# Kernel optimization log

Measured on AMD Instinct MI355X. Metric: run time of the kernel, lower is better.

The kernel has to match this reference:

```python
import jax, jax.numpy as jnp
import numpy as np

# Distance grid for SK tables: uniform, 512 points on [1.0, 10.0] Bohr (typical SKF grid)
NGRID = 512
X0 = 1.0
XMAX = 10.0
DX = (XMAX - X0) / (NGRID - 1)

E_EDGES = 2_000_000
N_NODES = 500_000
N_BOND_TYPES = 10
NUM_INGRLS = 16   # idp_sk.reduced_matrix_element
N_ATOM_TYPES = 4
N_ONSITE = 4


def setup_inputs() -> dict:
    key = jax.random.key(0)
    k1, k2, k3, k4, k5, k6 = jax.random.split(key, 6)
    # edge lengths inside the table range [X0, XMAX)
    rij = X0 + jax.random.uniform(k1, (E_EDGES,), dtype=jnp.float32) * (XMAX - X0 - 0.1)
    edge_type = jax.random.randint(k2, (E_EDGES,), 0, N_BOND_TYPES, dtype=jnp.int32)
    atom_type = jax.random.randint(k3, (N_NODES,), 0, N_ATOM_TYPES, dtype=jnp.int32)
    hopping_tables = jax.random.normal(k4, (N_BOND_TYPES, NUM_INGRLS, NGRID), dtype=jnp.float32)
    overlap_tables = jax.random.normal(k5, (N_BOND_TYPES, NUM_INGRLS, NGRID), dtype=jnp.float32)
    onsiteE = jax.random.normal(k6, (N_ATOM_TYPES, N_ONSITE), dtype=jnp.float32)
    return {"rij": rij, "edge_type": edge_type, "atom_type": atom_type,
            "hopping_tables": hopping_tables, "overlap_tables": overlap_tables,
            "onsiteE": onsiteE}


def _interp_tables(tables, etype, r):
    """1D linear interpolation (HoppingIntp method='linear'), vectorized over
    ALL edges at once instead of the per-bond-type masked loop.
    tables: [B, M, G]; etype: [E] int; r: [E] float -> [E, M]."""
    t = (r - X0) / DX
    i0 = jnp.clip(jnp.floor(t).astype(jnp.int32), 0, NGRID - 2)
    frac = (t - i0.astype(r.dtype))[:, None]          # [E, 1]
    y0 = tables[etype, :, i0]                          # [E, M] gather
    y1 = tables[etype, :, i0 + 1]                      # [E, M] gather
    return y0 * (1.0 - frac) + y1 * frac


def reference(rij, edge_type, atom_type, hopping_tables, overlap_tables, onsiteE):
    # edge SK hopping integrals: data[EDGE_FEATURES] = hopping_fn.get_skhij(rij, yy=hoptable)
    edge_features = _interp_tables(hopping_tables, edge_type, rij)     # [E, M]
    # edge SK overlap integrals (overlap=True branch)
    edge_overlap = _interp_tables(overlap_tables, edge_type, rij)      # [E, M]
    # onsite energies: onsite_fn.get_skEs(atomic_numbers) -> table lookup per atom
    node_features = onsiteE[atom_type]                                  # [N, n_onsite]
    return edge_features, edge_overlap, node_features
```

## Files before the change

kernel.cpp:

```cpp
#include <hip/hip_runtime.h>


#define NGRID 512
#define NUM_INGRLS 16
#define N_BOND_TYPES 10
#define PACKED_FLOATS (N_BOND_TYPES * NGRID * 32)
#define PACKED_BYTES  (PACKED_FLOATS * sizeof(float))

typedef float fx4 __attribute__((ext_vector_type(4)));

__global__ __launch_bounds__(256) void repack_tables(
    const float* __restrict__ hop,
    const float* __restrict__ ovl,
    float* __restrict__ packed)
{
    int t = blockIdx.x * blockDim.x + threadIdx.x;
    if (t >= N_BOND_TYPES * NGRID * NUM_INGRLS) return;
    int m = t & (NUM_INGRLS - 1);
    int g = (t >> 4) & (NGRID - 1);
    int b = t >> 13;
    float h = hop[((size_t)b * NUM_INGRLS + m) * NGRID + g];
    float o = ovl[((size_t)b * NUM_INGRLS + m) * NGRID + g];
    size_t row = ((size_t)b * NGRID + g) * 32;
    packed[row + m]      = h;
    packed[row + 16 + m] = o;
}

__global__ __launch_bounds__(256) void dftb_edge_packed_q(
    const float* __restrict__ rij,
    const int*   __restrict__ etype,
    const float* __restrict__ packed,
    float* __restrict__ out_hop,
    float* __restrict__ out_ovl,
    int E)
{
    const float X0f = 1.0f;
    const float DXf = (float)((10.0 - 1.0) / (NGRID - 1));

    int tid = blockIdx.x * blockDim.x + threadIdx.x;
    int e = tid >> 2;
    int q = tid & 3;
    if (e >= E) return;

    float r = rij[e];
    int   b = etype[e];

    float t  = (r - X0f) / DXf;
    int   i0 = (int)floorf(t);
    i0 = min(max(i0, 0), NGRID - 2);
    float frac = t - (float)i0;
    float w0   = 1.0f - frac;

    const fx4* row = (const fx4*)(packed + ((size_t)b * NGRID + i0) * 32);
    fx4 h0 = row[q];
    fx4 o0 = row[4 + q];
    fx4 h1 = row[8 + q];
    fx4 o1 = row[12 + q];

    fx4 hv = h0 * w0 + h1 * frac;
    fx4 ov = o0 * w0 + o1 * frac;

    size_t slot = (size_t)e * 4 + q;
    __builtin_nontemporal_store(hv, (fx4*)out_hop + slot);
    __builtin_nontemporal_store(ov, (fx4*)out_ovl + slot);
}

__global__ __launch_bounds__(256) void dftb_edge_kernel(
    const float* __restrict__ rij,
    const int*   __restrict__ etype,
    const float* __restrict__ hop,
    const float* __restrict__ ovl,
    float* __restrict__ out_hop,
    float* __restrict__ out_ovl,
    int E)
{
    const float X0f = 1.0f;
    const float DXf = (float)((10.0 - 1.0) / (NGRID - 1));

    int e = blockIdx.x * blockDim.x + threadIdx.x;
    if (e >= E) return;

    float r = rij[e];
    int   b = etype[e];

    float t  = (r - X0f) / DXf;
    int   i0 = (int)floorf(t);
    i0 = min(max(i0, 0), NGRID - 2);
    float frac = t - (float)i0;
    float w0   = 1.0f - frac;

    const float* hbase = hop + (size_t)b * (NUM_INGRLS * NGRID) + i0;
    const float* obase = ovl + (size_t)b * (NUM_INGRLS * NGRID) + i0;

    float oh[NUM_INGRLS];
    float oo[NUM_INGRLS];
#pragma unroll
    for (int m = 0; m < NUM_INGRLS; ++m) {
        float y0 = hbase[m * NGRID];
        float y1 = hbase[m * NGRID + 1];
        oh[m] = y0 * w0 + y1 * frac;
        float z0 = obase[m * NGRID];
        float z1 = obase[m * NGRID + 1];
        oo[m] = z0 * w0 + z1 * frac;
    }

    float4* oh4 = (float4*)(out_hop + (size_t)e * NUM_INGRLS);
    float4* oo4 = (float4*)(out_ovl + (size_t)e * NUM_INGRLS);
#pragma unroll
    for (int qq = 0; qq < 4; ++qq) {
        oh4[qq] = make_float4(oh[4*qq+0], oh[4*qq+1], oh[4*qq+2], oh[4*qq+3]);
        oo4[qq] = make_float4(oo[4*qq+0], oo[4*qq+1], oo[4*qq+2], oo[4*qq+3]);
    }
}

__global__ __launch_bounds__(256) void dftb_node_kernel(
    const int*   __restrict__ atype,
    const float* __restrict__ onsiteE,
    float* __restrict__ out,
    int N)
{
    int n = blockIdx.x * blockDim.x + threadIdx.x;
    if (n >= N) return;
    int a = atype[n];
    const float4* src = (const float4*)onsiteE;
    ((float4*)out)[n] = src[a];
}

extern "C" void kernel_launch(void* const* d_in, const int* in_sizes, int n_in,
                              void* d_out, int out_size, void* d_ws, size_t ws_size,
                              hipStream_t stream) {
    const float* rij       = (const float*)d_in[0];
    const int*   edge_type = (const int*)  d_in[1];
    const int*   atom_type = (const int*)  d_in[2];
    const float* hop_tab   = (const float*)d_in[3];
    const float* ovl_tab   = (const float*)d_in[4];
    const float* onsiteE   = (const float*)d_in[5];

    const int E = in_sizes[0];
    const int N = in_sizes[2];

    float* out_hop  = (float*)d_out;
    float* out_ovl  = out_hop + (size_t)E * NUM_INGRLS;
    float* out_node = out_ovl + (size_t)E * NUM_INGRLS;

    if (d_ws != nullptr && ws_size >= PACKED_BYTES) {
        float* packed = (float*)d_ws;
        {
            int total = N_BOND_TYPES * NGRID * NUM_INGRLS;
            dim3 block(256);
            dim3 grid((total + 255) / 256);
            repack_tables<<<grid, block, 0, stream>>>(hop_tab, ovl_tab, packed);
        }
        {
            long long total = 4LL * E;
            dim3 block(256);
            dim3 grid((unsigned)((total + 255) / 256));
            dftb_edge_packed_q<<<grid, block, 0, stream>>>(
                rij, edge_type, packed, out_hop, out_ovl, E);
        }
    } else {
        dim3 block(256);
        dim3 grid((E + 255) / 256);
        dftb_edge_kernel<<<grid, block, 0, stream>>>(
            rij, edge_type, hop_tab, ovl_tab, out_hop, out_ovl, E);
    }

    {
        dim3 block(256);
        dim3 grid((N + 255) / 256);
        dftb_node_kernel<<<grid, block, 0, stream>>>(
            atom_type, onsiteE, out_node, N);
    }
}
```

Baseline: 305.2 us.

## Pack SK tables as fp16 with adjacent grid endpoints per row

Repacks hopping and overlap tables into fp16 with each integral's g and g+1 values for both tables stored together. Each edge then fetches one contiguous row instead of two float rows. Work is split across 8 threads per edge with 2-float stores. The aim is to cut gather traffic and table footprint, at the cost of fp16 precision in the interpolated tables and narrower stores.

```diff
diff --git a/kernel.cpp b/kernel.cpp
--- a/kernel.cpp
+++ b/kernel.cpp
@@ -4,32 +4,40 @@
 #define NGRID 512
 #define NUM_INGRLS 16
 #define N_BOND_TYPES 10
-#define PACKED_FLOATS (N_BOND_TYPES * NGRID * 32)
-#define PACKED_BYTES  (PACKED_FLOATS * sizeof(float))
+#define PACK2_HALFS (N_BOND_TYPES * NGRID * NUM_INGRLS * 4)
+#define PACK2_BYTES (PACK2_HALFS * 2)
 
-typedef float fx4 __attribute__((ext_vector_type(4)));
+typedef float    fx4 __attribute__((ext_vector_type(4)));
+typedef float    fx2 __attribute__((ext_vector_type(2)));
+typedef _Float16 hx4 __attribute__((ext_vector_type(4)));
+typedef _Float16 hx8 __attribute__((ext_vector_type(8)));
 
-__global__ __launch_bounds__(256) void repack_tables(
+__global__ __launch_bounds__(256) void repack_tables_p2(
     const float* __restrict__ hop,
     const float* __restrict__ ovl,
-    float* __restrict__ packed)
+    _Float16* __restrict__ packed)
 {
     int t = blockIdx.x * blockDim.x + threadIdx.x;
     if (t >= N_BOND_TYPES * NGRID * NUM_INGRLS) return;
     int m = t & (NUM_INGRLS - 1);
     int g = (t >> 4) & (NGRID - 1);
     int b = t >> 13;
-    float h = hop[((size_t)b * NUM_INGRLS + m) * NGRID + g];
-    float o = ovl[((size_t)b * NUM_INGRLS + m) * NGRID + g];
-    size_t row = ((size_t)b * NGRID + g) * 32;
-    packed[row + m]      = h;
-    packed[row + 16 + m] = o;
+    int g1 = min(g + 1, NGRID - 1);
+    const float* hb = hop + ((size_t)b * NUM_INGRLS + m) * NGRID;
+    const float* ob = ovl + ((size_t)b * NUM_INGRLS + m) * NGRID;
+    hx4 v;
+    v[0] = (_Float16)hb[g];
+    v[1] = (_Float16)hb[g1];
+    v[2] = (_Float16)ob[g];
+    v[3] = (_Float16)ob[g1];
+    size_t idx = (((size_t)b * NGRID + g) * NUM_INGRLS + m) * 4;
+    *(hx4*)(packed + idx) = v;
 }
 
-__global__ __launch_bounds__(256) void dftb_edge_packed_q(
+__global__ __launch_bounds__(256) void dftb_edge_p2(
     const float* __restrict__ rij,
     const int*   __restrict__ etype,
-    const float* __restrict__ packed,
+    const _Float16* __restrict__ packed,
     float* __restrict__ out_hop,
     float* __restrict__ out_ovl,
     int E)
@@ -38,8 +46,8 @@
     const float DXf = (float)((10.0 - 1.0) / (NGRID - 1));
 
     int tid = blockIdx.x * blockDim.x + threadIdx.x;
-    int e = tid >> 2;
-    int q = tid & 3;
+    int e = tid >> 3;
+    int l = tid & 7;
     if (e >= E) return;
 
     float r = rij[e];
@@ -51,18 +59,18 @@
     float frac = t - (float)i0;
     float w0   = 1.0f - frac;
 
-    const fx4* row = (const fx4*)(packed + ((size_t)b * NGRID + i0) * 32);
-    fx4 h0 = row[q];
-    fx4 o0 = row[4 + q];
-    fx4 h1 = row[8 + q];
-    fx4 o1 = row[12 + q];
+    const hx8* src = (const hx8*)(packed + ((size_t)b * NGRID + i0) * (NUM_INGRLS * 4)) + l;
+    hx8 v = *src;
 
-    fx4 hv = h0 * w0 + h1 * frac;
-    fx4 ov = o0 * w0 + o1 * frac;
+    fx2 hv, ov;
+    hv[0] = (float)v[0] * w0 + (float)v[1] * frac;
+    ov[0] = (float)v[2] * w0 + (float)v[3] * frac;
+    hv[1] = (float)v[4] * w0 + (float)v[5] * frac;
+    ov[1] = (float)v[6] * w0 + (float)v[7] * frac;
 
-    size_t slot = (size_t)e * 4 + q;
-    __builtin_nontemporal_store(hv, (fx4*)out_hop + slot);
-    __builtin_nontemporal_store(ov, (fx4*)out_ovl + slot);
+    size_t slot = (size_t)e * 8 + l;
+    __builtin_nontemporal_store(hv, (fx2*)out_hop + slot);
+    __builtin_nontemporal_store(ov, (fx2*)out_ovl + slot);
 }
 
 __global__ __launch_bounds__(256) void dftb_edge_kernel(
@@ -143,19 +151,19 @@
     float* out_ovl  = out_hop + (size_t)E * NUM_INGRLS;
     float* out_node = out_ovl + (size_t)E * NUM_INGRLS;
 
-    if (d_ws != nullptr && ws_size >= PACKED_BYTES) {
-        float* packed = (float*)d_ws;
+    if (d_ws != nullptr && ws_size >= PACK2_BYTES) {
+        _Float16* packed = (_Float16*)d_ws;
         {
             int total = N_BOND_TYPES * NGRID * NUM_INGRLS;
             dim3 block(256);
             dim3 grid((total + 255) / 256);
-            repack_tables<<<grid, block, 0, stream>>>(hop_tab, ovl_tab, packed);
+            repack_tables_p2<<<grid, block, 0, stream>>>(hop_tab, ovl_tab, packed);
         }
         {
-            long long total = 4LL * E;
+            long long total = 8LL * E;
             dim3 block(256);
             dim3 grid((unsigned)((total + 255) / 256));
-            dftb_edge_packed_q<<<grid, block, 0, stream>>>(
+            dftb_edge_p2<<<grid, block, 0, stream>>>(
                 rij, edge_type, packed, out_hop, out_ovl, E);
         }
     } else {
```

Measured after the change: 308.0 us. About the same (+0.9%).
